# Optimization experiments

Hardware: AMD Instinct MI355X
Metric: run time of the kernel (lower is better)

The kernel has to match this reference:

```python
import jax, jax.numpy as jnp
import numpy as np

K = 3  # torch_geometric knn_interpolate default
EPS = 1e-16


def knn_interpolate(l_y, l_pos, h_pos):
    # squared distances [N_h, N_l]
    d2 = jnp.sum((h_pos[:, None, :] - l_pos[None, :, :]) ** 2, axis=-1)
    neg_d, idx = jax.lax.top_k(-d2, K)          # k nearest: idx [N_h, K]
    w = 1.0 / jnp.maximum(-neg_d, EPS)           # inverse squared-distance weights
    feats = l_y[idx]                             # [N_h, K, F] gather
    return jnp.sum(w[..., None] * feats, axis=1) / jnp.sum(w, axis=1, keepdims=True)


def mlp(x, W1, b1, W2, b2, W3, b3):
    x = jax.nn.relu(x @ W1 + b1)
    x = jax.nn.relu(x @ W2 + b2)
    return x @ W3 + b3


def setup_inputs() -> dict:
    key = jax.random.key(0)
    ks = jax.random.split(key, 8)
    N_h, N_l, H, O = 32768, 8192, 512, 128
    s1 = 1.0 / np.sqrt(H)
    return {
        "emb": jax.random.normal(ks[0], (N_h, H), jnp.float32),
        "l_y": jax.random.normal(ks[1], (N_l, O), jnp.float32),
        "l_pos": jax.random.uniform(ks[2], (N_l, 3), jnp.float32),
        "h_pos": jax.random.uniform(ks[3], (N_h, 3), jnp.float32),
        "W1": jax.random.normal(ks[4], (H, H), jnp.float32) * s1,
        "b1": jnp.zeros((H,), jnp.float32),
        "W2": jax.random.normal(ks[5], (H, H), jnp.float32) * s1,
        "b2": jnp.zeros((H,), jnp.float32),
        "W3": jax.random.normal(ks[6], (H, O), jnp.float32) * s1,
        "b3": jnp.zeros((O,), jnp.float32),
    }


def reference(emb, l_y, l_pos, h_pos, W1, b1, W2, b2, W3, b3):
    x = mlp(emb, W1, b1, W2, b2, W3, b3)
    return x + knn_interpolate(l_y, l_pos, h_pos)
```

## Files before the change

kernel.cpp:

```cpp
#include <hip/hip_runtime.h>
#include <stdint.h>

typedef __attribute__((ext_vector_type(4))) float f32x4;
typedef __attribute__((ext_vector_type(8))) short bf16x8;
typedef __attribute__((ext_vector_type(4))) unsigned short u16x4;

#define AS1(p) ((const __attribute__((address_space(1))) void*)(p))
#define AS3(p) ((__attribute__((address_space(3))) void*)(p))

__device__ __forceinline__ unsigned short f2bf(float f){
  unsigned u = __builtin_bit_cast(unsigned, f);
  u += 0x7FFF + ((u >> 16) & 1);
  return (unsigned short)(u >> 16);
}

template<int N> __device__ __forceinline__ void waitcnt_vm(){
  if constexpr (N==0) asm volatile("s_waitcnt vmcnt(0)" ::: "memory");
  else if constexpr (N==2) asm volatile("s_waitcnt vmcnt(2)" ::: "memory");
  else if constexpr (N==3) asm volatile("s_waitcnt vmcnt(3)" ::: "memory");
  else if constexpr (N==4) asm volatile("s_waitcnt vmcnt(4)" ::: "memory");
  else if constexpr (N==6) asm volatile("s_waitcnt vmcnt(6)" ::: "memory");
}

__global__ __launch_bounds__(256) void k_transpose3(const float* __restrict__ W1,
                                                    const float* __restrict__ W2,
                                                    const float* __restrict__ W3,
                                                    unsigned short* __restrict__ W1t,
                                                    unsigned short* __restrict__ W2t,
                                                    unsigned short* __restrict__ W3t){
  const int z = blockIdx.z;
  const float* in; unsigned short* out; int R, C;
  if (z == 0){ in = W1; out = W1t; R = 512; C = 512; }
  else if (z == 1){ in = W2; out = W2t; R = 512; C = 512; }
  else { in = W3; out = W3t; R = 512; C = 128; if (blockIdx.x >= 4) return; }
  __shared__ float tile[32][33];
  int tx = threadIdx.x & 31, ty = threadIdx.x >> 5;
  int c0 = blockIdx.x*32, r0 = blockIdx.y*32;
  #pragma unroll
  for (int i = 0; i < 4; i++)
    tile[ty + i*8][tx] = in[(size_t)(r0 + ty + i*8)*C + c0 + tx];
  __syncthreads();
  #pragma unroll
  for (int i = 0; i < 4; i++)
    out[(size_t)(c0 + ty + i*8)*R + r0 + tx] = f2bf(tile[tx][ty + i*8]);
}

template<int BM, int NC, int TW, int MINW, bool AF32, bool RELU, bool OUTBF16, bool ADDOUT>
__global__ __launch_bounds__(TW, MINW) void k_gemm(const void* __restrict__ Av,
                                                   const unsigned short* __restrict__ Bt,
                                                   const float* __restrict__ bias,
                                                   void* __restrict__ out, int K){
  constexpr int WARPS_M = BM/64;
  constexpr int WARPS_N = (TW/64)/WARPS_M;
  constexpr int WN = NC/WARPS_N;
  constexpr int NI = WN/16;
  constexpr int IA = AF32 ? 0 : (BM*4)/TW;
  constexpr int IB = (NC*4)/TW;
  constexpr int LS = IA + IB;

  __shared__ short As[3][BM*32];
  __shared__ short Bs[3][NC*32];

  const int tid  = threadIdx.x;
  const int lane = tid & 63, wid = tid >> 6;
  const int wr = wid / WARPS_N, wc = wid % WARPS_N;
  const int l15 = lane & 15, lk = lane >> 4;
  const int bm = blockIdx.x, bn = blockIdx.y;

  const unsigned short* Bsrc[IB];
  #pragma unroll
  for (int q = 0; q < IB; q++){
    int row = q*(TW/4) + (tid >> 2);
    int ch  = (tid & 3) ^ ((row >> 1) & 3);
    Bsrc[q] = Bt + (size_t)bn*NC*K + (size_t)row*K + ch*8;
  }
  const unsigned short* Asrc16[IA > 0 ? IA : 1];
  if constexpr (!AF32){
    #pragma unroll
    for (int a = 0; a < IA; a++){
      int row = a*(TW/4) + (tid >> 2);
      int ch  = (tid & 3) ^ ((row >> 1) & 3);
      Asrc16[a] = (const unsigned short*)Av + (size_t)bm*BM*K + (size_t)row*K + ch*8;
    }
  }
  const float* A32 = (const float*)Av + (size_t)bm*BM*K + (size_t)(tid>>2)*K + (size_t)(tid&3)*8;
  const int woff = (tid >> 2)*32 + ((tid & 3) ^ (((tid >> 2) >> 1) & 3))*8;

#define STAGE_B(t_, bb_) do{ int k0_ = (t_) << 5; _Pragma("unroll") \
  for (int q = 0; q < IB; q++) \
    __builtin_amdgcn_global_load_lds(AS1(Bsrc[q] + k0_), AS3(&Bs[bb_][(q*(TW/4))*32 + tid*8]), 16, 0, 0); \
}while(0)
#define STAGE_A16(t_, bb_) do{ int k0_ = (t_) << 5; _Pragma("unroll") \
  for (int a = 0; a < IA; a++) \
    __builtin_amdgcn_global_load_lds(AS1(Asrc16[a] + k0_), AS3(&As[bb_][(a*(TW/4))*32 + tid*8]), 16, 0, 0); \
}while(0)
#define A_CONV_WRITE(bb_) do{ bf16x8 p_; _Pragma("unroll") \
  for (int j_ = 0; j_ < 4; j_++){ p_[j_] = (short)f2bf(ra0[j_]); p_[j_+4] = (short)f2bf(ra1[j_]); } \
  *(bf16x8*)&As[bb_][woff] = p_; \
}while(0)

  f32x4 acc[4][NI];
  #pragma unroll
  for (int i = 0; i < 4; i++)
    #pragma unroll
    for (int j = 0; j < NI; j++) acc[i][j] = (f32x4){0.f,0.f,0.f,0.f};

  const int nt = K >> 5;
  f32x4 ra0, ra1;

  if constexpr (AF32){
    ra0 = *(const f32x4*)(A32);
    ra1 = *(const f32x4*)(A32 + 4);
    STAGE_B(0, 0);
    STAGE_B(1, 1);
    waitcnt_vm<IB>();
    A_CONV_WRITE(0);
    asm volatile("s_waitcnt lgkmcnt(0)" ::: "memory");
  } else {
    STAGE_A16(0, 0); STAGE_B(0, 0);
    STAGE_A16(1, 1); STAGE_B(1, 1);
    waitcnt_vm<LS>();
  }
  __builtin_amdgcn_s_barrier();

  int b = 0;
  for (int t = 0; t < nt; ++t){
    bf16x8 af[4], bg[NI];
    #pragma unroll
    for (int i = 0; i < 4; i++){
      int R = wr*64 + i*16 + l15;
      af[i] = *(const bf16x8*)&As[b][R*32 + (lk ^ ((R >> 1) & 3))*8];
    }
    #pragma unroll
    for (int j = 0; j < NI; j++){
      int R = wc*WN + j*16 + l15;
      bg[j] = *(const bf16x8*)&Bs[b][R*32 + (lk ^ ((R >> 1) & 3))*8];
    }

    int b2 = b + 2; if (b2 >= 3) b2 -= 3;
    if constexpr (AF32){
      if (t + 1 < nt){
        int k1 = (t + 1) << 5;
        ra0 = *(const f32x4*)(A32 + k1);
        ra1 = *(const f32x4*)(A32 + k1 + 4);
      }
      if (t + 2 < nt) STAGE_B(t + 2, b2);
    } else {
      if (t + 2 < nt){ STAGE_A16(t + 2, b2); STAGE_B(t + 2, b2); }
    }

    __builtin_amdgcn_s_setprio(1);
    #pragma unroll
    for (int i = 0; i < 4; i++)
      #pragma unroll
      for (int j = 0; j < NI; j++)
        acc[i][j] = __builtin_amdgcn_mfma_f32_16x16x32_bf16(af[i], bg[j], acc[i][j], 0, 0, 0);
    __builtin_amdgcn_s_setprio(0);

    if (t + 2 < nt) waitcnt_vm<(AF32 ? IB : LS)>();
    else            waitcnt_vm<0>();
    if constexpr (AF32){
      if (t + 1 < nt){
        int wb = b + 1; if (wb >= 3) wb -= 3;
        A_CONV_WRITE(wb);
      }
    }
    asm volatile("s_waitcnt lgkmcnt(0)" ::: "memory");
    __builtin_amdgcn_s_barrier();
    b = (b + 1 == 3) ? 0 : b + 1;
  }
#undef STAGE_B
#undef STAGE_A16
#undef A_CONV_WRITE

  const int row0 = bm*BM + wr*64 + lk*4;
  const int col0 = bn*NC + wc*WN + l15;
  const int NOUT = NC*gridDim.y;
  #pragma unroll
  for (int i = 0; i < 4; i++){
    #pragma unroll
    for (int j = 0; j < NI; j++){
      int col = col0 + j*16;
      float bv = bias[col];
      #pragma unroll
      for (int r = 0; r < 4; r++){
        int row = row0 + i*16 + r;
        float v = acc[i][j][r] + bv;
        if (RELU) v = fmaxf(v, 0.f);
        if (ADDOUT) v = v + ((const float*)out)[(size_t)row*NOUT + col];
        if (OUTBF16) ((unsigned short*)out)[(size_t)row*NOUT + col] = f2bf(v);
        else         ((float*)out)[(size_t)row*NOUT + col] = v;
      }
    }
  }
}

#define GD 14
#define GD3 (GD*GD*GD)
#define NL 8192

__device__ __forceinline__ int cellcoord(float x){
  int c = (int)(x * (float)GD);
  return min(GD-1, max(0, c));
}

__global__ __launch_bounds__(64) void k_zero(int* __restrict__ p){
  #pragma unroll
  for (int i = 0; i < 16; i++)
    ((int4*)p)[threadIdx.x*16 + i] = (int4){0,0,0,0};
}

__global__ __launch_bounds__(256) void k_hist(const float* __restrict__ l_pos,
                                              int* __restrict__ hist){
  int i = blockIdx.x*256 + threadIdx.x;
  float x = l_pos[3*i], y = l_pos[3*i+1], z = l_pos[3*i+2];
  int c = (cellcoord(z)*GD + cellcoord(y))*GD + cellcoord(x);
  atomicAdd(&hist[c], 1);
}

__global__ __launch_bounds__(1024) void k_scan(const int* __restrict__ hist,
                                               int* __restrict__ cellStart,
                                               int* __restrict__ cursor){
  __shared__ int s[1024];
  int t = threadIdx.x;
  int4 v = ((const int4*)hist)[t];
  int sum = v.x + v.y + v.z + v.w;
  s[t] = sum;
  __syncthreads();
  for (int off = 1; off < 1024; off <<= 1){
    int val = (t >= off) ? s[t-off] : 0;
    __syncthreads();
    s[t] += val;
    __syncthreads();
  }
  int base = s[t] - sum;
  int4 cs;
  cs.x = base;
  cs.y = base + v.x;
  cs.z = base + v.x + v.y;
  cs.w = base + v.x + v.y + v.z;
  ((int4*)cellStart)[t] = cs;
  ((int4*)cursor)[t]    = cs;
}

__global__ __launch_bounds__(256) void k_scatter(const float* __restrict__ l_pos,
                                                 int* __restrict__ cursor,
                                                 float4* __restrict__ sorted){
  int i = blockIdx.x*256 + threadIdx.x;
  float x = l_pos[3*i], y = l_pos[3*i+1], z = l_pos[3*i+2];
  int c = (cellcoord(z)*GD + cellcoord(y))*GD + cellcoord(x);
  int slot = atomicAdd(&cursor[c], 1);
  float4 q; q.x = x; q.y = y; q.z = z; q.w = __int_as_float(i);
  sorted[slot] = q;
}

#define KNN_INS(dv, gi) \
  if (gi != i0 && gi != i1 && gi != i2 && \
      (dv < d2 || (dv == d2 && gi < i2))){ \
    if (dv < d1 || (dv == d1 && gi < i1)){ \
      d2 = d1; i2 = i1; \
      if (dv < d0 || (dv == d0 && gi < i0)){ d1 = d0; i1 = i0; d0 = dv; i0 = gi; } \
      else { d1 = dv; i1 = gi; } \
    } else { d2 = dv; i2 = gi; } \
  }

#define KNN_MERGE16() \
  _Pragma("unroll") \
  for (int m = 1; m < 16; m <<= 1){ \
    float e0 = __shfl_xor(d0, m), e1 = __shfl_xor(d1, m), e2 = __shfl_xor(d2, m); \
    int   j0 = __shfl_xor(i0, m), j1 = __shfl_xor(i1, m), j2 = __shfl_xor(i2, m); \
    KNN_INS(e0, j0); KNN_INS(e1, j1); KNN_INS(e2, j2); \
  }

__global__ __launch_bounds__(256) void k_knn_grid(const float* __restrict__ h_pos,
                                                  const int* __restrict__ cellStart,
                                                  const float4* __restrict__ sorted,
                                                  float* __restrict__ w,
                                                  int* __restrict__ idx){
  const int t = blockIdx.x*256 + threadIdx.x;
  const int h = t >> 4, sl = t & 15;
  const float hx = h_pos[3*h], hy = h_pos[3*h+1], hz = h_pos[3*h+2];
  const int cx = cellcoord(hx), cy = cellcoord(hy), cz = cellcoord(hz);
  const float cs = 1.0f/(float)GD;
  float d0 = 3e38f, d1 = 3e38f, d2 = 3e38f;
  int   i0 = 0x7fffffff, i1 = 0x7fffffff, i2 = 0x7fffffff;

  for (int ci = sl; ci < 27; ci += 16){
    int dz = ci/9 - 1, dy = (ci - (ci/9)*9)/3 - 1, dx = ci % 3 - 1;
    int zz = cz+dz, yy = cy+dy, xx = cx+dx;
    if ((unsigned)zz >= GD || (unsigned)yy >= GD || (unsigned)xx >= GD) continue;
    int c = (zz*GD + yy)*GD + xx;
    int p0 = cellStart[c], p1 = cellStart[c+1];
    for (int p = p0; p < p1; p++){
      float4 qq = sorted[p];
      float ddx = hx - qq.x, ddy = hy - qq.y, ddz = hz - qq.z;
      float d = fmaf(ddx, ddx, fmaf(ddy, ddy, ddz*ddz));
      int gi = __float_as_int(qq.w);
      KNN_INS(d, gi);
    }
  }
  KNN_MERGE16();

  for (int r = 2; r < GD; r++){
    int rp = r - 1;
    float B = 3e38f;
    if (cx - rp > 0)      B = fminf(B, hx - (float)(cx-rp)*cs);
    if (cx + rp + 1 < GD) B = fminf(B, (float)(cx+rp+1)*cs - hx);
    if (cy - rp > 0)      B = fminf(B, hy - (float)(cy-rp)*cs);
    if (cy + rp + 1 < GD) B = fminf(B, (float)(cy+rp+1)*cs - hy);
    if (cz - rp > 0)      B = fminf(B, hz - (float)(cz-rp)*cs);
    if (cz + rp + 1 < GD) B = fminf(B, (float)(cz+rp+1)*cs - hz);
    if (d2 <= B*B) break;

    int side = 2*r + 1, ss = side*side, tot = ss*side;
    for (int ci = sl; ci < tot; ci += 16){
      int dz = ci/ss - r;
      int rem = ci - (ci/ss)*ss;
      int dy = rem/side - r, dx = rem - (rem/side)*side - r;
      int adx = abs(dx), ady = abs(dy), adz = abs(dz);
      if (max(adx, max(ady, adz)) < r) continue;
      int zz = cz+dz, yy = cy+dy, xx = cx+dx;
      if ((unsigned)zz >= GD || (unsigned)yy >= GD || (unsigned)xx >= GD) continue;
      int c = (zz*GD + yy)*GD + xx;
      int p0 = cellStart[c], p1 = cellStart[c+1];
      for (int p = p0; p < p1; p++){
        float4 qq = sorted[p];
        float ddx = hx - qq.x, ddy = hy - qq.y, ddz = hz - qq.z;
        float d = fmaf(ddx, ddx, fmaf(ddy, ddy, ddz*ddz));
        int gi = __float_as_int(qq.w);
        KNN_INS(d, gi);
      }
    }
    KNN_MERGE16();
  }

  if (sl == 0){
    w[3*h+0] = 1.0f/fmaxf(d0, 1e-16f); idx[3*h+0] = i0;
    w[3*h+1] = 1.0f/fmaxf(d1, 1e-16f); idx[3*h+1] = i1;
    w[3*h+2] = 1.0f/fmaxf(d2, 1e-16f); idx[3*h+2] = i2;
  }
}

__global__ __launch_bounds__(256) void k_knn_gather(const float* __restrict__ w,
                                                    const int* __restrict__ idx,
                                                    const float* __restrict__ l_y,
                                                    float* __restrict__ out){
  const int t = blockIdx.x*256 + threadIdx.x;
  const int h = t >> 5, lane = t & 31;
  const float w0 = w[h*3+0], w1 = w[h*3+1], w2 = w[h*3+2];
  const int   j0 = idx[h*3+0], j1 = idx[h*3+1], j2 = idx[h*3+2];
  const f32x4* ly4 = (const f32x4*)l_y;
  f32x4 a = ly4[(size_t)j0*32 + lane]*w0
          + ly4[(size_t)j1*32 + lane]*w1
          + ly4[(size_t)j2*32 + lane]*w2;
  float inv = 1.0f/(w0 + w1 + w2);
  ((f32x4*)out)[(size_t)h*32 + lane] = a*inv;
}

extern "C" void kernel_launch(void* const* d_in, const int* in_sizes, int n_in,
                              void* d_out, int out_size, void* d_ws, size_t ws_size,
                              hipStream_t stream){
  const float* emb   = (const float*)d_in[0];
  const float* l_y   = (const float*)d_in[1];
  const float* l_pos = (const float*)d_in[2];
  const float* h_pos = (const float*)d_in[3];
  const float* W1    = (const float*)d_in[4];
  const float* b1    = (const float*)d_in[5];
  const float* W2    = (const float*)d_in[6];
  const float* b2    = (const float*)d_in[7];
  const float* W3    = (const float*)d_in[8];
  const float* b3    = (const float*)d_in[9];

  const int M = 32768, H = 512;

  char* ws = (char*)d_ws;
  unsigned short* bufA = (unsigned short*)(ws);
  unsigned short* bufB = (unsigned short*)(ws + 33554432);
  unsigned short* W1t  = (unsigned short*)(ws + 67108864);
  unsigned short* W2t  = (unsigned short*)(ws + 67633152);
  unsigned short* W3t  = (unsigned short*)(ws + 68157440);
  int*    hist      = (int*)   (ws + 68288512);
  int*    cellStart = (int*)   (ws + 68304896);
  int*    cursor    = (int*)   (ws + 68321280);
  float4* sorted    = (float4*)(ws + 68354048);
  float* wts = (float*)(ws + 74579968);
  int*   idx = (int*)  (ws + 74973184);

  k_transpose3<<<dim3(16, 16, 3), 256, 0, stream>>>(W1, W2, W3, W1t, W2t, W3t);

  k_zero<<<dim3(1), 64, 0, stream>>>(hist);
  k_hist<<<dim3(NL/256), 256, 0, stream>>>(l_pos, hist);
  k_scan<<<dim3(1), 1024, 0, stream>>>(hist, cellStart, cursor);
  k_scatter<<<dim3(NL/256), 256, 0, stream>>>(l_pos, cursor, sorted);
  k_knn_grid<<<dim3(M*16/256), 256, 0, stream>>>(h_pos, cellStart, sorted, wts, idx);
  k_knn_gather<<<dim3(M*32/256), 256, 0, stream>>>(wts, idx, l_y, (float*)d_out);

  k_gemm<128, 256, 512, 4, true,  true,  true,  false><<<dim3(M/128, 2), 512, 0, stream>>>(emb,  W1t, b1, bufB, H);
  k_gemm<128, 256, 512, 4, false, true,  true,  false><<<dim3(M/128, 2), 512, 0, stream>>>(bufB, W2t, b2, bufA, H);
  k_gemm<64,  128, 256, 2, false, false, false, true ><<<dim3(M/64,  1), 256, 0, stream>>>(bufA, W3t, b3, d_out, H);
}
```

Baseline: 120.0 us.

## Add 256x256 tiled GEMM for layer two and fuse grid build kernels

Adds a new bf16 MFMA GEMM kernel with 256x256 block tiles, a 4-stage LDS ring fed by direct global-to-LDS loads, and a split A-fragment schedule, then uses it for the second MLP layer. It also merges the four grid-construction kernels (zero, histogram, scan, scatter) into one single-block kernel that keeps the histogram and cursors in LDS. The larger tile is meant to raise operand reuse and cut global traffic for the middle GEMM. The merged build kernel removes three launches and global atomics, but it runs on only one workgroup and needs heavy LDS use per block.

New measurement: 123.8 us. 3.2% more time.

```diff
diff --git a/kernel.cpp b/kernel.cpp
--- a/kernel.cpp
+++ b/kernel.cpp
@@ -45,6 +45,118 @@
     out[(size_t)(c0 + ty + i*8)*R + r0 + tx] = f2bf(tile[tx][ty + i*8]);
 }
 
+template<bool RELU>
+__global__ __launch_bounds__(512, 2) void k_gemm256(const unsigned short* __restrict__ A,
+                                                    const unsigned short* __restrict__ Bt,
+                                                    const float* __restrict__ bias,
+                                                    unsigned short* __restrict__ out,
+                                                    int K, int N){
+  __shared__ short As[4][256*32];
+  __shared__ short Bs[4][256*32];
+  const int tid  = threadIdx.x;
+  const int lane = tid & 63;
+  const int wid  = tid >> 6;
+  const int wr = wid >> 2, wc = wid & 3;
+  const int l15 = lane & 15, lk = lane >> 4;
+  const int bm = blockIdx.x, bn = blockIdx.y;
+
+  const unsigned short* Asrc[2];
+  const unsigned short* Bsrc[2];
+  int dsto[2];
+  #pragma unroll
+  for (int u = 0; u < 2; u++){
+    int cp = u*512 + tid, r = cp >> 2, s = cp & 3;
+    int c  = s ^ ((r & 3) ^ ((r >> 2) & 3));
+    Asrc[u] = A  + (size_t)(bm*256 + r)*K + c*8;
+    Bsrc[u] = Bt + (size_t)(bn*256 + r)*K + c*8;
+    dsto[u] = cp*8;
+  }
+  int aoff[8], boff[4];
+  #pragma unroll
+  for (int rf = 0; rf < 8; rf++){
+    int R = wr*128 + rf*16 + l15;
+    aoff[rf] = R*32 + (lk ^ ((R & 3) ^ ((R >> 2) & 3)))*8;
+  }
+  #pragma unroll
+  for (int cf = 0; cf < 4; cf++){
+    int R = wc*64 + cf*16 + l15;
+    boff[cf] = R*32 + (lk ^ ((R & 3) ^ ((R >> 2) & 3)))*8;
+  }
+
+#define STG_U(t_, bb_, u_) do{ int k0_ = (t_) << 5; \
+  __builtin_amdgcn_global_load_lds(AS1(Asrc[u_] + k0_), AS3(&As[bb_][dsto[u_]]), 16, 0, 0); \
+  __builtin_amdgcn_global_load_lds(AS1(Bsrc[u_] + k0_), AS3(&Bs[bb_][dsto[u_]]), 16, 0, 0); \
+}while(0)
+
+  f32x4 acc[8][4];
+  #pragma unroll
+  for (int i = 0; i < 8; i++)
+    #pragma unroll
+    for (int j = 0; j < 4; j++) acc[i][j] = (f32x4){0.f,0.f,0.f,0.f};
+
+  const int nt = K >> 5;
+  STG_U(0, 0, 0); STG_U(0, 0, 1);
+  STG_U(1, 1, 0); STG_U(1, 1, 1);
+  waitcnt_vm<4>();
+  __builtin_amdgcn_s_barrier();
+
+  for (int t = 0; t < nt; ++t){
+    const int b  = t & 3;
+    const int b2 = (t + 2) & 3;
+    bf16x8 bg[4], af[4];
+    #pragma unroll
+    for (int cf = 0; cf < 4; cf++) bg[cf] = *(const bf16x8*)&Bs[b][boff[cf]];
+    #pragma unroll
+    for (int rf = 0; rf < 4; rf++) af[rf] = *(const bf16x8*)&As[b][aoff[rf]];
+    if (t + 2 < nt) STG_U(t + 2, b2, 0);
+    __builtin_amdgcn_s_barrier();
+    asm volatile("s_waitcnt lgkmcnt(0)" ::: "memory");
+    __builtin_amdgcn_s_setprio(1);
+    #pragma unroll
+    for (int rf = 0; rf < 4; rf++)
+      #pragma unroll
+      for (int cf = 0; cf < 4; cf++)
+        acc[rf][cf] = __builtin_amdgcn_mfma_f32_16x16x32_bf16(af[rf], bg[cf], acc[rf][cf], 0, 0, 0);
+    __builtin_amdgcn_s_setprio(0);
+    __builtin_amdgcn_s_barrier();
+    bf16x8 af2[4];
+    #pragma unroll
+    for (int rf = 0; rf < 4; rf++) af2[rf] = *(const bf16x8*)&As[b][aoff[rf + 4]];
+    if (t + 2 < nt) STG_U(t + 2, b2, 1);
+    __builtin_amdgcn_s_barrier();
+    asm volatile("s_waitcnt lgkmcnt(0)" ::: "memory");
+    __builtin_amdgcn_s_setprio(1);
+    #pragma unroll
+    for (int rf = 0; rf < 4; rf++)
+      #pragma unroll
+      for (int cf = 0; cf < 4; cf++)
+        acc[rf + 4][cf] = __builtin_amdgcn_mfma_f32_16x16x32_bf16(af2[rf], bg[cf], acc[rf + 4][cf], 0, 0, 0);
+    __builtin_amdgcn_s_setprio(0);
+    if (t + 2 < nt) waitcnt_vm<4>();
+    else            waitcnt_vm<0>();
+    __builtin_amdgcn_s_barrier();
+  }
+#undef STG_U
+
+  const int row0 = bm*256 + wr*128 + lk*4;
+  const int col0 = bn*256 + wc*64 + l15;
+  #pragma unroll
+  for (int rf = 0; rf < 8; rf++){
+    #pragma unroll
+    for (int cf = 0; cf < 4; cf++){
+      int col = col0 + cf*16;
+      float bv = bias[col];
+      #pragma unroll
+      for (int r = 0; r < 4; r++){
+        int row = row0 + rf*16 + r;
+        float v = acc[rf][cf][r] + bv;
+        if (RELU) v = fmaxf(v, 0.f);
+        out[(size_t)row*N + col] = f2bf(v);
+      }
+    }
+  }
+}
+
 template<int BM, int NC, int TW, int MINW, bool AF32, bool RELU, bool OUTBF16, bool ADDOUT>
 __global__ __launch_bounds__(TW, MINW) void k_gemm(const void* __restrict__ Av,
                                                    const unsigned short* __restrict__ Bt,
@@ -204,25 +316,23 @@
   return min(GD-1, max(0, c));
 }
 
-__global__ __launch_bounds__(64) void k_zero(int* __restrict__ p){
-  #pragma unroll
-  for (int i = 0; i < 16; i++)
-    ((int4*)p)[threadIdx.x*16 + i] = (int4){0,0,0,0};
-}
-
-__global__ __launch_bounds__(256) void k_hist(const float* __restrict__ l_pos,
-                                              int* __restrict__ hist){
-  int i = blockIdx.x*256 + threadIdx.x;
-  float x = l_pos[3*i], y = l_pos[3*i+1], z = l_pos[3*i+2];
-  int c = (cellcoord(z)*GD + cellcoord(y))*GD + cellcoord(x);
-  atomicAdd(&hist[c], 1);
-}
-
-__global__ __launch_bounds__(1024) void k_scan(const int* __restrict__ hist,
-                                               int* __restrict__ cellStart,
-                                               int* __restrict__ cursor){
+__global__ __launch_bounds__(1024) void k_grid_build(const float* __restrict__ l_pos,
+                                                     int* __restrict__ cellStart,
+                                                     float4* __restrict__ sorted){
+  __shared__ int hist[4096];
+  __shared__ int cur[4096];
   __shared__ int s[1024];
-  int t = threadIdx.x;
+  const int t = threadIdx.x;
+  ((int4*)hist)[t] = (int4){0,0,0,0};
+  __syncthreads();
+  #pragma unroll
+  for (int k = 0; k < 8; k++){
+    int i = k*1024 + t;
+    float x = l_pos[3*i], y = l_pos[3*i+1], z = l_pos[3*i+2];
+    int c = (cellcoord(z)*GD + cellcoord(y))*GD + cellcoord(x);
+    atomicAdd(&hist[c], 1);
+  }
+  __syncthreads();
   int4 v = ((const int4*)hist)[t];
   int sum = v.x + v.y + v.z + v.w;
   s[t] = sum;
@@ -240,18 +350,17 @@
   cs.z = base + v.x + v.y;
   cs.w = base + v.x + v.y + v.z;
   ((int4*)cellStart)[t] = cs;
-  ((int4*)cursor)[t]    = cs;
-}
-
-__global__ __launch_bounds__(256) void k_scatter(const float* __restrict__ l_pos,
-                                                 int* __restrict__ cursor,
-                                                 float4* __restrict__ sorted){
-  int i = blockIdx.x*256 + threadIdx.x;
-  float x = l_pos[3*i], y = l_pos[3*i+1], z = l_pos[3*i+2];
-  int c = (cellcoord(z)*GD + cellcoord(y))*GD + cellcoord(x);
-  int slot = atomicAdd(&cursor[c], 1);
-  float4 q; q.x = x; q.y = y; q.z = z; q.w = __int_as_float(i);
-  sorted[slot] = q;
+  ((int4*)cur)[t] = cs;
+  __syncthreads();
+  #pragma unroll
+  for (int k = 0; k < 8; k++){
+    int i = k*1024 + t;
+    float x = l_pos[3*i], y = l_pos[3*i+1], z = l_pos[3*i+2];
+    int c = (cellcoord(z)*GD + cellcoord(y))*GD + cellcoord(x);
+    int slot = atomicAdd(&cur[c], 1);
+    float4 q; q.x = x; q.y = y; q.z = z; q.w = __int_as_float(i);
+    sorted[slot] = q;
+  }
 }
 
 #define KNN_INS(dv, gi) \
@@ -379,23 +488,18 @@
   unsigned short* W1t  = (unsigned short*)(ws + 67108864);
   unsigned short* W2t  = (unsigned short*)(ws + 67633152);
   unsigned short* W3t  = (unsigned short*)(ws + 68157440);
-  int*    hist      = (int*)   (ws + 68288512);
   int*    cellStart = (int*)   (ws + 68304896);
-  int*    cursor    = (int*)   (ws + 68321280);
   float4* sorted    = (float4*)(ws + 68354048);
   float* wts = (float*)(ws + 74579968);
   int*   idx = (int*)  (ws + 74973184);
 
   k_transpose3<<<dim3(16, 16, 3), 256, 0, stream>>>(W1, W2, W3, W1t, W2t, W3t);
 
-  k_zero<<<dim3(1), 64, 0, stream>>>(hist);
-  k_hist<<<dim3(NL/256), 256, 0, stream>>>(l_pos, hist);
-  k_scan<<<dim3(1), 1024, 0, stream>>>(hist, cellStart, cursor);
-  k_scatter<<<dim3(NL/256), 256, 0, stream>>>(l_pos, cursor, sorted);
+  k_grid_build<<<dim3(1), 1024, 0, stream>>>(l_pos, cellStart, sorted);
   k_knn_grid<<<dim3(M*16/256), 256, 0, stream>>>(h_pos, cellStart, sorted, wts, idx);
   k_knn_gather<<<dim3(M*32/256), 256, 0, stream>>>(wts, idx, l_y, (float*)d_out);
 
   k_gemm<128, 256, 512, 4, true,  true,  true,  false><<<dim3(M/128, 2), 512, 0, stream>>>(emb,  W1t, b1, bufB, H);
-  k_gemm<128, 256, 512, 4, false, true,  true,  false><<<dim3(M/128, 2), 512, 0, stream>>>(bufB, W2t, b2, bufA, H);
+  k_gemm256<true><<<dim3(M/256, 2), 512, 0, stream>>>(bufB, W2t, b2, bufA, H, H);
   k_gemm<64,  128, 256, 2, false, false, false, true ><<<dim3(M/64,  1), 256, 0, stream>>>(bufA, W3t, b3, d_out, H);
 }
```

## Fuse grid build into weight-transpose kernel and fuse kNN search with gather

Applied to the files above, without the earlier changes.

The four small grid-building kernels (zero, histogram, scan, scatter) are folded into one extra z-slice of the weight transpose launch. That slice runs in a single block using shared-memory histogram and cursors. The kNN search kernel now does the weighted feature gather directly with its 16 lanes per point, which removes the intermediate weight/index buffers and one launch. The grid build becomes serialised in one block, which may lengthen the critical path. Each of the 16 lanes gathers two float4 per neighbour instead of one.

After: 119.8 us, median of 2. No clear change (-0.2%).

```diff
diff --git a/kernel.cpp b/kernel.cpp
--- a/kernel.cpp
+++ b/kernel.cpp
@@ -3,7 +3,6 @@
 
 typedef __attribute__((ext_vector_type(4))) float f32x4;
 typedef __attribute__((ext_vector_type(8))) short bf16x8;
-typedef __attribute__((ext_vector_type(4))) unsigned short u16x4;
 
 #define AS1(p) ((const __attribute__((address_space(1))) void*)(p))
 #define AS3(p) ((__attribute__((address_space(3))) void*)(p))
@@ -22,13 +21,69 @@
   else if constexpr (N==6) asm volatile("s_waitcnt vmcnt(6)" ::: "memory");
 }
 
-__global__ __launch_bounds__(256) void k_transpose3(const float* __restrict__ W1,
-                                                    const float* __restrict__ W2,
-                                                    const float* __restrict__ W3,
-                                                    unsigned short* __restrict__ W1t,
-                                                    unsigned short* __restrict__ W2t,
-                                                    unsigned short* __restrict__ W3t){
+#define GD 14
+#define NL 8192
+
+__device__ __forceinline__ int cellcoord(float x){
+  int c = (int)(x * (float)GD);
+  return min(GD-1, max(0, c));
+}
+
+__global__ __launch_bounds__(256) void k_pre(const float* __restrict__ W1,
+                                             const float* __restrict__ W2,
+                                             const float* __restrict__ W3,
+                                             unsigned short* __restrict__ W1t,
+                                             unsigned short* __restrict__ W2t,
+                                             unsigned short* __restrict__ W3t,
+                                             const float* __restrict__ l_pos,
+                                             int* __restrict__ cellStart,
+                                             float4* __restrict__ sorted){
   const int z = blockIdx.z;
+  if (z == 3){
+    if (blockIdx.x != 0 || blockIdx.y != 0) return;
+    __shared__ int hist[4096];
+    __shared__ int cur[4096];
+    __shared__ int s[256];
+    const int t = threadIdx.x;
+    #pragma unroll
+    for (int k = 0; k < 16; k++) hist[k*256 + t] = 0;
+    __syncthreads();
+    for (int k = 0; k < 32; k++){
+      int i = k*256 + t;
+      float x = l_pos[3*i], y = l_pos[3*i+1], zz = l_pos[3*i+2];
+      int c = (cellcoord(zz)*GD + cellcoord(y))*GD + cellcoord(x);
+      atomicAdd(&hist[c], 1);
+    }
+    __syncthreads();
+    int loc[16]; int sum = 0;
+    #pragma unroll
+    for (int e = 0; e < 16; e++){ loc[e] = hist[t*16 + e]; sum += loc[e]; }
+    s[t] = sum;
+    __syncthreads();
+    for (int off = 1; off < 256; off <<= 1){
+      int val = (t >= off) ? s[t-off] : 0;
+      __syncthreads();
+      s[t] += val;
+      __syncthreads();
+    }
+    int base = s[t] - sum;
+    #pragma unroll
+    for (int e = 0; e < 16; e++){
+      cellStart[t*16 + e] = base;
+      cur[t*16 + e] = base;
+      base += loc[e];
+    }
+    __syncthreads();
+    for (int k = 0; k < 32; k++){
+      int i = k*256 + t;
+      float x = l_pos[3*i], y = l_pos[3*i+1], zz = l_pos[3*i+2];
+      int c = (cellcoord(zz)*GD + cellcoord(y))*GD + cellcoord(x);
+      int slot = atomicAdd(&cur[c], 1);
+      float4 q; q.x = x; q.y = y; q.z = zz; q.w = __int_as_float(i);
+      sorted[slot] = q;
+    }
+    return;
+  }
   const float* in; unsigned short* out; int R, C;
   if (z == 0){ in = W1; out = W1t; R = 512; C = 512; }
   else if (z == 1){ in = W2; out = W2t; R = 512; C = 512; }
@@ -195,65 +250,6 @@
   }
 }
 
-#define GD 14
-#define GD3 (GD*GD*GD)
-#define NL 8192
-
-__device__ __forceinline__ int cellcoord(float x){
-  int c = (int)(x * (float)GD);
-  return min(GD-1, max(0, c));
-}
-
-__global__ __launch_bounds__(64) void k_zero(int* __restrict__ p){
-  #pragma unroll
-  for (int i = 0; i < 16; i++)
-    ((int4*)p)[threadIdx.x*16 + i] = (int4){0,0,0,0};
-}
-
-__global__ __launch_bounds__(256) void k_hist(const float* __restrict__ l_pos,
-                                              int* __restrict__ hist){
-  int i = blockIdx.x*256 + threadIdx.x;
-  float x = l_pos[3*i], y = l_pos[3*i+1], z = l_pos[3*i+2];
-  int c = (cellcoord(z)*GD + cellcoord(y))*GD + cellcoord(x);
-  atomicAdd(&hist[c], 1);
-}
-
-__global__ __launch_bounds__(1024) void k_scan(const int* __restrict__ hist,
-                                               int* __restrict__ cellStart,
-                                               int* __restrict__ cursor){
-  __shared__ int s[1024];
-  int t = threadIdx.x;
-  int4 v = ((const int4*)hist)[t];
-  int sum = v.x + v.y + v.z + v.w;
-  s[t] = sum;
-  __syncthreads();
-  for (int off = 1; off < 1024; off <<= 1){
-    int val = (t >= off) ? s[t-off] : 0;
-    __syncthreads();
-    s[t] += val;
-    __syncthreads();
-  }
-  int base = s[t] - sum;
-  int4 cs;
-  cs.x = base;
-  cs.y = base + v.x;
-  cs.z = base + v.x + v.y;
-  cs.w = base + v.x + v.y + v.z;
-  ((int4*)cellStart)[t] = cs;
-  ((int4*)cursor)[t]    = cs;
-}
-
-__global__ __launch_bounds__(256) void k_scatter(const float* __restrict__ l_pos,
-                                                 int* __restrict__ cursor,
-                                                 float4* __restrict__ sorted){
-  int i = blockIdx.x*256 + threadIdx.x;
-  float x = l_pos[3*i], y = l_pos[3*i+1], z = l_pos[3*i+2];
-  int c = (cellcoord(z)*GD + cellcoord(y))*GD + cellcoord(x);
-  int slot = atomicAdd(&cursor[c], 1);
-  float4 q; q.x = x; q.y = y; q.z = z; q.w = __int_as_float(i);
-  sorted[slot] = q;
-}
-
 #define KNN_INS(dv, gi) \
   if (gi != i0 && gi != i1 && gi != i2 && \
       (dv < d2 || (dv == d2 && gi < i2))){ \
@@ -272,11 +268,11 @@
     KNN_INS(e0, j0); KNN_INS(e1, j1); KNN_INS(e2, j2); \
   }
 
-__global__ __launch_bounds__(256) void k_knn_grid(const float* __restrict__ h_pos,
-                                                  const int* __restrict__ cellStart,
-                                                  const float4* __restrict__ sorted,
-                                                  float* __restrict__ w,
-                                                  int* __restrict__ idx){
+__global__ __launch_bounds__(256) void k_knn(const float* __restrict__ h_pos,
+                                             const int* __restrict__ cellStart,
+                                             const float4* __restrict__ sorted,
+                                             const float* __restrict__ l_y,
+                                             float* __restrict__ out){
   const int t = blockIdx.x*256 + threadIdx.x;
   const int h = t >> 4, sl = t & 15;
   const float hx = h_pos[3*h], hy = h_pos[3*h+1], hz = h_pos[3*h+2];
@@ -334,27 +330,19 @@
     KNN_MERGE16();
   }
 
-  if (sl == 0){
-    w[3*h+0] = 1.0f/fmaxf(d0, 1e-16f); idx[3*h+0] = i0;
-    w[3*h+1] = 1.0f/fmaxf(d1, 1e-16f); idx[3*h+1] = i1;
-    w[3*h+2] = 1.0f/fmaxf(d2, 1e-16f); idx[3*h+2] = i2;
-  }
-}
-
-__global__ __launch_bounds__(256) void k_knn_gather(const float* __restrict__ w,
-                                                    const int* __restrict__ idx,
-                                                    const float* __restrict__ l_y,
-                                                    float* __restrict__ out){
-  const int t = blockIdx.x*256 + threadIdx.x;
-  const int h = t >> 5, lane = t & 31;
-  const float w0 = w[h*3+0], w1 = w[h*3+1], w2 = w[h*3+2];
-  const int   j0 = idx[h*3+0], j1 = idx[h*3+1], j2 = idx[h*3+2];
+  float w0 = 1.0f/fmaxf(d0, 1e-16f);
+  float w1 = 1.0f/fmaxf(d1, 1e-16f);
+  float w2 = 1.0f/fmaxf(d2, 1e-16f);
+  float inv = 1.0f/(w0 + w1 + w2);
   const f32x4* ly4 = (const f32x4*)l_y;
-  f32x4 a = ly4[(size_t)j0*32 + lane]*w0
-          + ly4[(size_t)j1*32 + lane]*w1
-          + ly4[(size_t)j2*32 + lane]*w2;
-  float inv = 1.0f/(w0 + w1 + w2);
-  ((f32x4*)out)[(size_t)h*32 + lane] = a*inv;
+  size_t b0 = (size_t)i0*32 + sl*2;
+  size_t b1 = (size_t)i1*32 + sl*2;
+  size_t b2 = (size_t)i2*32 + sl*2;
+  f32x4 a0 = ly4[b0]*w0     + ly4[b1]*w1     + ly4[b2]*w2;
+  f32x4 a1 = ly4[b0 + 1]*w0 + ly4[b1 + 1]*w1 + ly4[b2 + 1]*w2;
+  size_t o = (size_t)h*32 + sl*2;
+  ((f32x4*)out)[o]     = a0*inv;
+  ((f32x4*)out)[o + 1] = a1*inv;
 }
 
 extern "C" void kernel_launch(void* const* d_in, const int* in_sizes, int n_in,
@@ -379,21 +367,13 @@
   unsigned short* W1t  = (unsigned short*)(ws + 67108864);
   unsigned short* W2t  = (unsigned short*)(ws + 67633152);
   unsigned short* W3t  = (unsigned short*)(ws + 68157440);
-  int*    hist      = (int*)   (ws + 68288512);
   int*    cellStart = (int*)   (ws + 68304896);
-  int*    cursor    = (int*)   (ws + 68321280);
   float4* sorted    = (float4*)(ws + 68354048);
-  float* wts = (float*)(ws + 74579968);
-  int*   idx = (int*)  (ws + 74973184);
-
-  k_transpose3<<<dim3(16, 16, 3), 256, 0, stream>>>(W1, W2, W3, W1t, W2t, W3t);
-
-  k_zero<<<dim3(1), 64, 0, stream>>>(hist);
-  k_hist<<<dim3(NL/256), 256, 0, stream>>>(l_pos, hist);
-  k_scan<<<dim3(1), 1024, 0, stream>>>(hist, cellStart, cursor);
-  k_scatter<<<dim3(NL/256), 256, 0, stream>>>(l_pos, cursor, sorted);
-  k_knn_grid<<<dim3(M*16/256), 256, 0, stream>>>(h_pos, cellStart, sorted, wts, idx);
-  k_knn_gather<<<dim3(M*32/256), 256, 0, stream>>>(wts, idx, l_y, (float*)d_out);
+
+  k_pre<<<dim3(16, 16, 4), 256, 0, stream>>>(W1, W2, W3, W1t, W2t, W3t,
+                                             l_pos, cellStart, sorted);
+
+  k_knn<<<dim3(M*16/256), 256, 0, stream>>>(h_pos, cellStart, sorted, l_y, (float*)d_out);
 
   k_gemm<128, 256, 512, 4, true,  true,  true,  false><<<dim3(M/128, 2), 512, 0, stream>>>(emb,  W1t, b1, bufB, H);
   k_gemm<128, 256, 512, 4, false, true,  true,  false><<<dim3(M/128, 2), 512, 0, stream>>>(bufB, W2t, b2, bufA, H);
```
